# Kernel optimization log

Measured on AMD Instinct MI355X. Metric: run time of the kernel, lower is better.

The kernel has to match this reference:

```python
import jax, jax.numpy as jnp
import numpy as np
import math

N, S, R = 1, 128, 256
CM, CZ, C, MSA_H, PAIR_H, CTM, FF = 256, 128, 32, 8, 4, 128, 4
SCALE = 1.0 / math.sqrt(C)


def _ln(x, w, b):
    m = jnp.mean(x, -1, keepdims=True)
    v = jnp.var(x, -1, keepdims=True)
    return (x - m) / jnp.sqrt(v + 1e-5) * w + b


def _gated_attn(x, gate_w, qkv_w, out_w, head, bias=None):
    # x: [n, s, r, cin]; attention over r within each (n, s, head)
    n, s, r, _ = x.shape
    gate = jax.nn.sigmoid(x @ gate_w).reshape(n, s, r, head, C)
    qkv = (x @ qkv_w).reshape(n, s, r, 3, head, C)
    q, k, v = qkv[..., 0, :, :], qkv[..., 1, :, :], qkv[..., 2, :, :]
    sim = jax.nn.softmax(jnp.einsum('nsqhc,nskhc->nshqk', q, k) * SCALE, axis=-1)
    if bias is not None:
        sim = sim + bias  # NOTE: source adds bias AFTER softmax; kept faithful
    att = jnp.einsum('nshqk,nskhc->nsqhc', sim, v) * gate
    return att.reshape(n, s, r, head * C) @ out_w


def _tri_mul(x, n1w, n1b, n2w, n2b, p1, p2, p3, p4, p5, p6, incoming):
    xn = _ln(x, n1w, n1b)
    a = jax.nn.sigmoid(xn @ p1) * (xn @ p2)
    b = jax.nn.sigmoid(xn @ p3) * (xn @ p4)
    if incoming:
        p = jnp.einsum('nrsk,nrtk->nstk', a, b)
        g = jnp.swapaxes(jax.nn.sigmoid(xn @ p6), 1, 2)
    else:
        p = jnp.einsum('nsrk,ntrk->nstk', a, b)
        g = jax.nn.sigmoid(xn @ p6)
    return (_ln(p, n2w, n2b) @ p5) * g


def setup_inputs() -> dict:
    keys = iter(jax.random.split(jax.random.key(0), 80))

    def rn(shape, scale=0.02):
        return jax.random.normal(next(keys), shape, dtype=jnp.float32) * scale

    ones = lambda n: jnp.ones((n,), jnp.float32)
    zeros = lambda n: jnp.zeros((n,), jnp.float32)
    d = dict(
        msa_repr=rn((N, S, R, CM), 1.0),
        pair_repr=rn((N, R, R, CZ), 1.0),
        row_norm_m_w=ones(CM), row_norm_m_b=zeros(CM),
        row_norm_z_w=ones(CZ), row_norm_z_b=zeros(CZ),
        row_gate=rn((CM, MSA_H * C)), row_qkv=rn((CM, 3 * MSA_H * C)),
        row_out=rn((MSA_H * C, CM)), row_bias=rn((CZ, MSA_H)),
        col_norm_w=ones(CM), col_norm_b=zeros(CM),
        col_gate=rn((CM, MSA_H * C)), col_qkv=rn((CM, 3 * MSA_H * C)),
        col_out=rn((MSA_H * C, CM)),
        mt_norm_w=ones(CM), mt_norm_b=zeros(CM),
        mt_p1=rn((CM, FF * CM)), mt_p2=rn((FF * CM, CM)),
        outer_norm_w=ones(CM), outer_norm_b=zeros(CM),
        outer_p1=rn((CM, C)), outer_p2=rn((CM, C)), outer_out=rn((C * C, CZ)),
        tmo_n1_w=ones(CZ), tmo_n1_b=zeros(CZ), tmo_n2_w=ones(CTM), tmo_n2_b=zeros(CTM),
        tmo_p1=rn((CZ, CTM)), tmo_p2=rn((CZ, CTM)), tmo_p3=rn((CZ, CTM)), tmo_p4=rn((CZ, CTM)),
        tmo_p5=rn((CTM, CZ)), tmo_p6=rn((CZ, CZ)),
        tmi_n1_w=ones(CZ), tmi_n1_b=zeros(CZ), tmi_n2_w=ones(CTM), tmi_n2_b=zeros(CTM),
        tmi_p1=rn((CZ, CTM)), tmi_p2=rn((CZ, CTM)), tmi_p3=rn((CZ, CTM)), tmi_p4=rn((CZ, CTM)),
        tmi_p5=rn((CTM, CZ)), tmi_p6=rn((CZ, CZ)),
        tas_norm_w=ones(CZ), tas_norm_b=zeros(CZ),
        tas_gate=rn((CZ, PAIR_H * C)), tas_qkv=rn((CZ, 3 * PAIR_H * C)),
        tas_out=rn((PAIR_H * C, CZ)), tas_bias=rn((CZ, PAIR_H)),
        tae_norm_w=ones(CZ), tae_norm_b=zeros(CZ),
        tae_gate=rn((CZ, PAIR_H * C)), tae_qkv=rn((CZ, 3 * PAIR_H * C)),
        tae_out=rn((PAIR_H * C, CZ)), tae_bias=rn((CZ, PAIR_H)),
        pt_norm_w=ones(CZ), pt_norm_b=zeros(CZ),
        pt_p1=rn((CZ, FF * CZ)), pt_p2=rn((FF * CZ, CZ)),
    )
    return d


def reference(msa_repr, pair_repr, row_norm_m_w, row_norm_m_b, row_norm_z_w, row_norm_z_b, row_gate, row_qkv, row_out, row_bias, col_norm_w, col_norm_b, col_gate, col_qkv, col_out, mt_norm_w, mt_norm_b, mt_p1, mt_p2, outer_norm_w, outer_norm_b, outer_p1, outer_p2, outer_out, tmo_n1_w, tmo_n1_b, tmo_n2_w, tmo_n2_b, tmo_p1, tmo_p2, tmo_p3, tmo_p4, tmo_p5, tmo_p6, tmi_n1_w, tmi_n1_b, tmi_n2_w, tmi_n2_b, tmi_p1, tmi_p2, tmi_p3, tmi_p4, tmi_p5, tmi_p6, tas_norm_w, tas_norm_b, tas_gate, tas_qkv, tas_out, tas_bias, tae_norm_w, tae_norm_b, tae_gate, tae_qkv, tae_out, tae_bias, pt_norm_w, pt_norm_b, pt_p1, pt_p2):
    msa, pair = msa_repr, pair_repr
    # 1. MSA row attention with pair bias
    xm = _ln(msa, row_norm_m_w, row_norm_m_b)
    xz = _ln(pair, row_norm_z_w, row_norm_z_b)
    bias = jnp.transpose(xz @ row_bias, (0, 3, 1, 2))[:, None]  # [N,1,H,R,R]
    msa = msa + _gated_attn(xm, row_gate, row_qkv, row_out, MSA_H, bias)
    # 2. MSA column attention
    xm = _ln(msa, col_norm_w, col_norm_b)
    msa = msa + jnp.swapaxes(_gated_attn(jnp.swapaxes(xm, 1, 2), col_gate, col_qkv, col_out, MSA_H), 1, 2)
    # 3. MSA transition
    xm = _ln(msa, mt_norm_w, mt_norm_b)
    msa = msa + jax.nn.relu(xm @ mt_p1) @ mt_p2
    # 4. outer product mean (no division in source; sum over s)
    xm = _ln(msa, outer_norm_w, outer_norm_b)
    a = jnp.swapaxes(xm @ outer_p1, 1, 2)  # [n,r,s,c]
    b = jnp.swapaxes(xm @ outer_p2, 1, 2)  # [n,t,s,c]
    outer = jnp.einsum('nrsc,ntse->nrtce', a, b).reshape(a.shape[0], a.shape[1], b.shape[1], C * C)
    pair = pair + outer @ outer_out
    # 5/6. triangle multiplicative updates (outgoing then incoming)
    pair = pair + _tri_mul(pair, tmo_n1_w, tmo_n1_b, tmo_n2_w, tmo_n2_b, tmo_p1, tmo_p2, tmo_p3, tmo_p4, tmo_p5, tmo_p6, False)
    pair = pair + _tri_mul(pair, tmi_n1_w, tmi_n1_b, tmi_n2_w, tmi_n2_b, tmi_p1, tmi_p2, tmi_p3, tmi_p4, tmi_p5, tmi_p6, True)
    # 7. triangle attention (node start)
    xz = _ln(pair, tas_norm_w, tas_norm_b)
    bias = jnp.transpose(xz @ tas_bias, (0, 1, 3, 2))[:, :, :, None, :]  # [N,S,H,1,R]
    pair = pair + _gated_attn(xz, tas_gate, tas_qkv, tas_out, PAIR_H, bias)
    # 8. triangle attention (node end): transpose residue axes
    xz = jnp.swapaxes(_ln(pair, tae_norm_w, tae_norm_b), 1, 2)
    bias = jnp.transpose(xz @ tae_bias, (0, 1, 3, 2))[:, :, :, None, :]
    pair = pair + jnp.swapaxes(_gated_attn(xz, tae_gate, tae_qkv, tae_out, PAIR_H, bias), 1, 2)
    # 9. pair transition
    xz = _ln(pair, pt_norm_w, pt_norm_b)
    pair = pair + jax.nn.relu(xz @ pt_p1) @ pt_p2
    return msa, pair
```

## Files before the change

kernel.cpp:

```cpp
#include <hip/hip_runtime.h>
#include <hip/hip_bf16.h>
#include <stdint.h>

typedef __hip_bfloat16 bf16;
typedef __attribute__((ext_vector_type(4))) int   i32x4;
typedef __attribute__((ext_vector_type(4))) float f32x4;


__device__ __forceinline__ float toF(float x){ return x; }
__device__ __forceinline__ float toF(bf16 x){ return __bfloat162float(x); }
__device__ __forceinline__ bf16  toB(float x){ return __float2bfloat16(x); }

__device__ __forceinline__ void gload16(const bf16* g, bf16* l){
    __builtin_amdgcn_global_load_lds((const __attribute__((address_space(1))) void*)g,
                                     (__attribute__((address_space(3))) void*)l, 16, 0, 0);
}

#define NW_IN 58
struct WStage {
    const void* src[NW_IN];
    int off[NW_IN];
    int K[NW_IN], N[NW_IN];
};
__global__ __launch_bounds__(256) void cvt_all_k(WStage t, bf16* __restrict__ base,
                                                 const uint32_t* __restrict__ probe){
    bool isbf = (probe[0] == 0x3F803F80u);
    const int wi = blockIdx.y;
    const void* in = t.src[wi];
    bf16* out = base + t.off[wi];
    const int K = t.K[wi], N = t.N[wi];
    const int total = K ? K*N : N;
    for (int i = blockIdx.x*256 + threadIdx.x; i < total; i += gridDim.x*256){
        float v = isbf ? toF(((const bf16*)in)[i]) : ((const float*)in)[i];
        if (K){ int k = i / N, n = i - k*N; out[(size_t)n*K + k] = toB(v); }
        else    out[i] = toB(v);
    }
}
__global__ void in2f_k(const void* __restrict__ in, float* __restrict__ out, int n,
                       const uint32_t* __restrict__ probe){
    bool isbf = (probe[0] == 0x3F803F80u);
    int i = blockIdx.x*256 + threadIdx.x;
    if (i < n) out[i] = isbf ? toF(((const bf16*)in)[i]) : ((const float*)in)[i];
}

template<typename T>
__global__ void ln_k(const T* __restrict__ x, const bf16* __restrict__ w, const bf16* __restrict__ b,
                     bf16* __restrict__ out, int D){
    int row = blockIdx.x, c = threadIdx.x;
    float v = toF(x[(size_t)row*D + c]);
    float s1 = v, s2 = v*v;
    #pragma unroll
    for (int o=32;o>0;o>>=1){ s1 += __shfl_down(s1,o); s2 += __shfl_down(s2,o); }
    __shared__ float r1[4], r2[4];
    int lane = c & 63, wid = c >> 6;
    if (lane==0){ r1[wid]=s1; r2[wid]=s2; }
    __syncthreads();
    int nw = blockDim.x >> 6;
    float m=0.f, q=0.f;
    for (int i=0;i<nw;i++){ m+=r1[i]; q+=r2[i]; }
    m /= (float)D; q = q/(float)D - m*m;
    float inv = rsqrtf(q + 1e-5f);
    out[(size_t)row*D + c] = toB((v-m)*inv*toF(w[c]) + toF(b[c]));
}

template<int MODE, int HN>
__global__ __launch_bounds__(256) void bproj_k(const bf16* __restrict__ xz, const bf16* __restrict__ Wb,
                                               float* __restrict__ outb){
    __shared__ float WbS[128*HN];
    const int i = blockIdx.x, t = threadIdx.x;
    for (int idx = t; idx < 128*HN; idx += 256) WbS[idx] = toF(Wb[idx]);
    __syncthreads();
    const bf16* row = xz + ((size_t)i*256 + t)*128;
    float d[HN] = {};
    #pragma unroll 4
    for (int c8 = 0; c8 < 16; ++c8){
        uint4 v = *(const uint4*)(row + c8*8);
        bf16 tmp[8]; *(uint4*)tmp = v;
        #pragma unroll
        for (int u=0;u<8;u++){
            float x = toF(tmp[u]);
            #pragma unroll
            for (int h=0;h<HN;h++) d[h] += x * WbS[(c8*8+u)*HN + h];
        }
    }
    #pragma unroll
    for (int h=0;h<HN;h++){
        size_t idx = (MODE==0) ? ((size_t)h*65536 + (size_t)i*256 + t)
                   : (MODE==1) ? ((size_t)(i*HN+h)*256 + t)
                               : ((size_t)(t*HN+h)*256 + i);
        outb[idx] = d[h];
    }
}

template<int ACT, int MUL, int RES, int HM>
__global__ __launch_bounds__(256) void mgemm_k(const bf16* __restrict__ A, const bf16* __restrict__ Bt,
                                               bf16* __restrict__ C, float* __restrict__ Res,
                                               const bf16* __restrict__ Mul,
                                               int M, int N, int K, int lda, size_t astep,
                                               int ldbt, size_t ldc, int res_off, int gtrans){
    __shared__ alignas(16) bf16 As[128*32];
    __shared__ alignas(16) bf16 Bs[128*32];
    const int tid  = threadIdx.x;
    const int m0   = blockIdx.y << 7, n0 = blockIdx.x << 7;
    const int lane = tid & 63, w = tid >> 6;
    const int wr   = (w >> 1) << 6, wc = (w & 1) << 6;
    const int fr   = lane & 15, fq = lane >> 4;
    const int sr = tid >> 2, sc = (tid & 3) << 3;
    const bf16* ga = A  + (size_t)(m0 + sr)*lda  + sc;
    const bf16* gb = Bt + (size_t)(n0 + sr)*ldbt + sc;
    bf16* la = As + tid*8;
    bf16* lb = Bs + tid*8;
    const size_t gaS = (size_t)64*lda, gbS = (size_t)64*ldbt;

    f32x4 acc[4][4] = {};
    for (int k0=0; k0<K; k0+=32){
        gload16(ga, la);        gload16(ga + gaS, la + 2048);
        gload16(gb, lb);        gload16(gb + gbS, lb + 2048);
        ga += astep; gb += 32;
        __syncthreads();
        i32x4 af[4], bv[4];
        #pragma unroll
        for (int i=0;i<4;i++) af[i] = *(const i32x4*)(As + ((wr + i*16 + fr) << 5) + (fq << 3));
        #pragma unroll
        for (int j=0;j<4;j++) bv[j] = *(const i32x4*)(Bs + ((wc + j*16 + fr) << 5) + (fq << 3));
        #pragma unroll
        for (int i=0;i<4;i++)
            #pragma unroll
            for (int j=0;j<4;j++)
                asm("v_mfma_f32_16x16x32_bf16 %0, %1, %2, %0"
                    : "+v"(acc[i][j]) : "v"(af[i]), "v"(bv[j]));
        __syncthreads();
    }
    #pragma unroll
    for (int i=0;i<4;i++){
        const int mB = m0 + wr + i*16 + (fq << 2);
        #pragma unroll
        for (int j=0;j<4;j++){
            const int n = n0 + wc + j*16 + fr;
            #pragma unroll
            for (int r=0;r<4;r++){
                int m = mB + r;
                float x = acc[i][j][r];
                if (ACT==1) x = 1.f/(1.f + __expf(-x));
                else if (ACT==2) x = fmaxf(x, 0.f);
                if (MUL){
                    int mr = gtrans ? (((m & 255) << 8) | (m >> 8)) : m;
                    x *= toF(Mul[(size_t)mr*N + n]);
                }
                if (RES) Res[(size_t)(m + res_off)*N + n] += x;
                else if (HM) C[(size_t)(n>>5)*ldc + (size_t)m*32 + (n&31)] = toB(x);
                else     C[(size_t)m*ldc + n] = toB(x);
            }
        }
    }
}

template<int ACT, int MUL, int RES, int GATE, int MHM>
__global__ __launch_bounds__(256) void sgemm_k(const bf16* __restrict__ A,
        const bf16* __restrict__ Bt1, const bf16* __restrict__ Bt2,
        bf16* __restrict__ C, float* __restrict__ Res, const bf16* __restrict__ Mul,
        int M, int lda, int ldbt, int ldc, size_t ldmul, int res_off, int gtrans){
    __shared__ alignas(16) bf16 Bs1[128*128];
    __shared__ alignas(16) bf16 Bs2[GATE ? 128*128 : 16];
    const int tid = threadIdx.x;
    for (int idx = tid; idx < 2048; idx += 256){
        int n = idx >> 4, cc = idx & 15;
        int sc = (cc ^ (n & 15)) << 3;
        *(uint4*)(Bs1 + n*128 + sc) = *(const uint4*)(Bt1 + (size_t)n*ldbt + (cc<<3));
        if (GATE)
            *(uint4*)(Bs2 + n*128 + sc) = *(const uint4*)(Bt2 + (size_t)n*ldbt + (cc<<3));
    }
    __syncthreads();
    const int lane = tid & 63, w = tid >> 6;
    const int fr = lane & 15, fq = lane >> 4;
    const int mb = blockIdx.x*128 + w*32;
    f32x4 acc[2][8] = {};
    f32x4 acc2[2][8] = {};
    #pragma unroll
    for (int k0=0;k0<4;k0++){
        i32x4 af[2];
        #pragma unroll
        for (int i=0;i<2;i++)
            af[i] = *(const i32x4*)(A + (size_t)(mb + i*16 + fr)*lda + k0*32 + fq*8);
        const int co = ((k0*4 + fq) ^ fr) << 3;
        #pragma unroll
        for (int j=0;j<8;j++){
            i32x4 bf1 = *(const i32x4*)(Bs1 + (j*16+fr)*128 + co);
            #pragma unroll
            for (int i=0;i<2;i++)
                asm("v_mfma_f32_16x16x32_bf16 %0, %1, %2, %0"
                    : "+v"(acc[i][j]) : "v"(af[i]), "v"(bf1));
            if (GATE){
                i32x4 bf2 = *(const i32x4*)(Bs2 + (j*16+fr)*128 + co);
                #pragma unroll
                for (int i=0;i<2;i++)
                    asm("v_mfma_f32_16x16x32_bf16 %0, %1, %2, %0"
                        : "+v"(acc2[i][j]) : "v"(af[i]), "v"(bf2));
            }
        }
    }
    #pragma unroll
    for (int i=0;i<2;i++){
        #pragma unroll
        for (int j=0;j<8;j++){
            const int n = j*16 + fr;
            #pragma unroll
            for (int r=0;r<4;r++){
                int m = mb + i*16 + (fq<<2) + r;
                float x = acc[i][j][r];
                if (GATE) x = acc2[i][j][r] / (1.f + __expf(-x));
                else if (ACT==1) x = 1.f/(1.f + __expf(-x));
                else if (ACT==2) x = fmaxf(x, 0.f);
                if (MUL){
                    int mr = gtrans ? (((m & 255) << 8) | (m >> 8)) : m;
                    if (MHM) x *= toF(Mul[(size_t)(n>>5)*ldmul + (size_t)mr*32 + (n&31)]);
                    else     x *= toF(Mul[(size_t)mr*ldmul + n]);
                }
                if (RES) Res[(size_t)(m + res_off)*128 + n] += x;
                else     C[(size_t)m*ldc + n] = toB(x);
            }
        }
    }
}

__global__ __launch_bounds__(256) void btrimul_k(const bf16* __restrict__ aT, const bf16* __restrict__ bT,
                                                 bf16* __restrict__ pT){
    __shared__ alignas(16) bf16 As[128*32];
    __shared__ alignas(16) bf16 Bs[128*32];
    const int tid  = threadIdx.x;
    const int m0   = blockIdx.y << 7, n0 = blockIdx.x << 7;
    const size_t zb = (size_t)blockIdx.z << 16;
    const int lane = tid & 63, w = tid >> 6;
    const int wr   = (w >> 1) << 6, wc = (w & 1) << 6;
    const int fr   = lane & 15, fq = lane >> 4;
    const int sr = tid >> 2, sc = (tid & 3) << 3;
    const bf16* ga = aT + zb + (size_t)(m0 + sr)*256 + sc;
    const bf16* gb = bT + zb + (size_t)(n0 + sr)*256 + sc;
    bf16* la = As + tid*8;
    bf16* lb = Bs + tid*8;
    const size_t gS = (size_t)64*256;

    f32x4 acc[4][4] = {};
    for (int k0=0; k0<256; k0+=32){
        gload16(ga, la);        gload16(ga + gS, la + 2048);
        gload16(gb, lb);        gload16(gb + gS, lb + 2048);
        ga += 32; gb += 32;
        __syncthreads();
        i32x4 af[4], bv[4];
        #pragma unroll
        for (int i=0;i<4;i++) af[i] = *(const i32x4*)(As + ((wr + i*16 + fr) << 5) + (fq << 3));
        #pragma unroll
        for (int j=0;j<4;j++) bv[j] = *(const i32x4*)(Bs + ((wc + j*16 + fr) << 5) + (fq << 3));
        #pragma unroll
        for (int i=0;i<4;i++)
            #pragma unroll
            for (int j=0;j<4;j++)
                asm("v_mfma_f32_16x16x32_bf16 %0, %1, %2, %0"
                    : "+v"(acc[i][j]) : "v"(af[i]), "v"(bv[j]));
        __syncthreads();
    }
    #pragma unroll
    for (int i=0;i<4;i++){
        const int mB = m0 + wr + i*16 + (fq << 2);
        #pragma unroll
        for (int j=0;j<4;j++){
            const int n = n0 + wc + j*16 + fr;
            #pragma unroll
            for (int r=0;r<4;r++)
                pT[zb + (size_t)(mB + r)*256 + n] = toB(acc[i][j][r]);
        }
    }
}

__global__ __launch_bounds__(256) void rc2k_k(const bf16* __restrict__ in, bf16* __restrict__ out, int swap){
    __shared__ uint16_t T[128][137];
    const int tt = blockIdx.x, tid = threadIdx.x;
    size_t base_pp, out_off; int ppstride;
    if (!swap){ base_pp = (size_t)tt*128;                  ppstride = 1;   out_off = (size_t)tt*128; }
    else      { int J = tt>>1, I0 = (tt&1)*128;
                base_pp = (size_t)I0*256 + J;              ppstride = 256; out_off = (size_t)J*256 + I0; }
    for (int it=0; it<8; ++it){
        int idx = tid + it*256;
        int r = idx >> 4, c8 = (idx & 15) << 3;
        uint4 v = *(const uint4*)(in + (base_pp + (size_t)r*ppstride)*128 + c8);
        uint16_t tmp[8]; *(uint4*)tmp = v;
        #pragma unroll
        for (int t=0;t<8;t++) T[r][c8+t] = tmp[t];
    }
    __syncthreads();
    for (int it=0; it<8; ++it){
        int idx = tid + it*256;
        int k = idx >> 4, r8 = (idx & 15) << 3;
        uint16_t tmp[8];
        #pragma unroll
        for (int t=0;t<8;t++) tmp[t] = T[r8+t][k];
        *(uint4*)(out + (size_t)k*65536 + out_off + r8) = *(uint4*)tmp;
    }
}
__global__ __launch_bounds__(256) void k2rc_k(const bf16* __restrict__ in, bf16* __restrict__ out){
    __shared__ uint16_t T[128][137];
    const int tt = blockIdx.x, tid = threadIdx.x;
    const size_t a0 = (size_t)tt*128;
    for (int it=0; it<8; ++it){
        int idx = tid + it*256;
        int k = idx >> 4, r8 = (idx & 15) << 3;
        uint4 v = *(const uint4*)(in + (size_t)k*65536 + a0 + r8);
        uint16_t tmp[8]; *(uint4*)tmp = v;
        #pragma unroll
        for (int t=0;t<8;t++) T[r8+t][k] = tmp[t];
    }
    __syncthreads();
    for (int it=0; it<8; ++it){
        int idx = tid + it*256;
        int r = idx >> 4, c8 = (idx & 15) << 3;
        uint16_t tmp[8];
        #pragma unroll
        for (int t=0;t<8;t++) tmp[t] = T[r][c8+t];
        *(uint4*)(out + (a0 + r)*128 + c8) = *(uint4*)tmp;
    }
}

template<int ACT, int MUL, int RES>
__global__ __launch_bounds__(256) void gemm_k(const bf16* __restrict__ A, const bf16* __restrict__ Bw,
                                              bf16* __restrict__ C, float* __restrict__ Res,
                                              const bf16* __restrict__ Mul,
                                              int M, int N, int K, int ldb, int res_off, int gtrans){
    __shared__ float As[64][33];
    __shared__ float Bs[32][65];
    int tid = threadIdx.x;
    int m0 = blockIdx.y*64, n0 = blockIdx.x*64;
    int tx = tid & 15, ty = tid >> 4;
    float acc[4][4] = {};
    for (int k0=0; k0<K; k0+=32){
        for (int i=tid; i<64*32; i+=256){
            int r = i>>5, cc = i&31;
            As[r][cc] = toF(A[(size_t)(m0+r)*K + k0 + cc]);
        }
        for (int i=tid; i<32*64; i+=256){
            int r = i>>6, cc = i&63; int col = n0+cc;
            Bs[r][cc] = (col < N) ? toF(Bw[(size_t)(k0+r)*ldb + col]) : 0.f;
        }
        __syncthreads();
        #pragma unroll 8
        for (int k=0;k<32;k++){
            float a4[4], b4[4];
            #pragma unroll
            for (int i=0;i<4;i++) a4[i] = As[ty*4+i][k];
            #pragma unroll
            for (int j=0;j<4;j++) b4[j] = Bs[k][tx*4+j];
            #pragma unroll
            for (int i=0;i<4;i++)
                #pragma unroll
                for (int j=0;j<4;j++) acc[i][j] += a4[i]*b4[j];
        }
        __syncthreads();
    }
    #pragma unroll
    for (int i=0;i<4;i++){
        int m = m0 + ty*4 + i;
        #pragma unroll
        for (int j=0;j<4;j++){
            int n = n0 + tx*4 + j;
            if (n >= N) continue;
            float x = acc[i][j];
            if (ACT==1) x = 1.f/(1.f + __expf(-x));
            else if (ACT==2) x = fmaxf(x, 0.f);
            if (MUL){
                int mr = gtrans ? (((m & 255) << 8) | (m >> 8)) : m;
                x *= toF(Mul[(size_t)mr*N + n]);
            }
            if (RES) Res[(size_t)(m + res_off)*N + n] += x;
            else     C[(size_t)m*N + n] = toB(x);
        }
    }
}

template<int BIAS, int L>
__global__ __launch_bounds__(256) void attn4_k(bf16* __restrict__ QO,
                                               const bf16* __restrict__ Kp, const bf16* __restrict__ Vp,
                                               const float* __restrict__ bias,
                                               int H, size_t HS, int sO, int sL){
    constexpr int MW  = L/4;
    constexpr int IFR = MW/16;
    constexpr int KC  = 32;
    constexpr int NCH = L/KC;
    constexpr int VP  = L + 8;
    __shared__ alignas(16) bf16 VT_lds[32*VP];
    __shared__ alignas(16) bf16 P_lds[L*40];
    __shared__ float red[8*32 + 32];
    const int o = blockIdx.y, h = blockIdx.x, tid = threadIdx.x;
    const int lane = tid & 63, w = tid >> 6;
    const int fr = lane & 15, fq = lane >> 4;
    const size_t hb = (size_t)h*HS;

    for (int idx = tid; idx < L*4; idx += 256){
        int l = idx >> 2, c8 = (idx & 3) << 3;
        size_t p = hb + (size_t)(o*sO + l*sL)*32 + c8;
        uint4 vv = *(const uint4*)(Vp + p);
        bf16 tmp[8]; *(uint4*)tmp = vv;
        #pragma unroll
        for (int t=0;t<8;t++) VT_lds[(c8+t)*VP + l] = tmp[t];
    }
    __syncthreads();

    float* ObS = red + 256;
    if (BIAS == 2){
        int c = tid & 31, g = tid >> 5;
        const float* bp = bias + (size_t)(o*H + h)*256;
        float p = 0.f;
        for (int k = g*(L/8); k < (g+1)*(L/8); ++k)
            p += bp[k] * toF(VT_lds[c*VP + k]);
        red[g*32 + c] = p;
        __syncthreads();
        if (tid < 32){
            float s = 0.f;
            #pragma unroll
            for (int g2=0; g2<8; ++g2) s += red[g2*32 + tid];
            ObS[tid] = s;
        }
        __syncthreads();
    }

    i32x4 qf[IFR];
    #pragma unroll
    for (int i=0;i<IFR;i++){
        int q = w*MW + i*16 + fr;
        qf[i] = *(const i32x4*)(QO + hb + (size_t)(o*sO + q*sL)*32 + fq*8);
    }
    const bf16* kbase = Kp + hb + (size_t)o*sO*32 + fq*8 + (size_t)fr*sL*32;
    const size_t kstep = (size_t)sL*32;

    bf16* Pw = P_lds + w*MW*40;
    f32x4 accO[IFR][2] = {};
    f32x4 accB[IFR][2] = {};
    float lsum[IFR][4] = {};

    for (int ch=0; ch<NCH; ++ch){
        const int k0 = ch*KC;
        f32x4 sa[IFR][2] = {};
        i32x4 kf[2];
        #pragma unroll
        for (int j=0;j<2;j++) kf[j] = *(const i32x4*)(kbase + (size_t)(k0 + j*16)*kstep);
        #pragma unroll
        for (int i=0;i<IFR;i++)
            #pragma unroll
            for (int j=0;j<2;j++)
                asm("v_mfma_f32_16x16x32_bf16 %0, %1, %2, %0"
                    : "+v"(sa[i][j]) : "v"(qf[i]), "v"(kf[j]));
        #pragma unroll
        for (int i=0;i<IFR;i++)
            #pragma unroll
            for (int j=0;j<2;j++)
                #pragma unroll
                for (int r=0;r<4;r++){
                    float e = __expf(sa[i][j][r] * 0.17677669529663687f);
                    lsum[i][r] += e;
                    Pw[(i*16 + fq*4 + r)*40 + j*16 + fr] = toB(e);
                }
        i32x4 vf[2];
        #pragma unroll
        for (int j=0;j<2;j++) vf[j] = *(const i32x4*)(VT_lds + (j*16 + fr)*VP + k0 + fq*8);
        #pragma unroll
        for (int i=0;i<IFR;i++){
            i32x4 pa = *(const i32x4*)(Pw + (i*16 + fr)*40 + fq*8);
            #pragma unroll
            for (int j=0;j<2;j++)
                asm("v_mfma_f32_16x16x32_bf16 %0, %1, %2, %0"
                    : "+v"(accO[i][j]) : "v"(pa), "v"(vf[j]));
        }
        if (BIAS == 1){
            #pragma unroll
            for (int it=0; it<32; ++it){
                int q = it*2 + (lane>>5), kk = lane&31;
                Pw[q*40 + kk] = toB(bias[(size_t)h*65536 + (size_t)(w*MW + q)*256 + k0 + kk]);
            }
            #pragma unroll
            for (int i=0;i<IFR;i++){
                i32x4 pa = *(const i32x4*)(Pw + (i*16 + fr)*40 + fq*8);
                #pragma unroll
                for (int j=0;j<2;j++)
                    asm("v_mfma_f32_16x16x32_bf16 %0, %1, %2, %0"
                        : "+v"(accB[i][j]) : "v"(pa), "v"(vf[j]));
            }
        }
    }
    #pragma unroll
    for (int i=0;i<IFR;i++)
        #pragma unroll
        for (int r=0;r<4;r++){
            float s = lsum[i][r];
            s += __shfl_xor(s, 1); s += __shfl_xor(s, 2);
            s += __shfl_xor(s, 4); s += __shfl_xor(s, 8);
            lsum[i][r] = 1.f / s;
        }
    #pragma unroll
    for (int i=0;i<IFR;i++)
        #pragma unroll
        for (int j=0;j<2;j++)
            #pragma unroll
            for (int r=0;r<4;r++){
                int q = w*MW + i*16 + fq*4 + r;
                int c = j*16 + fr;
                float v = accO[i][j][r]*lsum[i][r];
                if (BIAS==1) v += accB[i][j][r];
                if (BIAS==2) v += ObS[c];
                QO[hb + (size_t)(o*sO + q*sL)*32 + c] = toB(v);
            }
}

__global__ void mulsigHM_k(bf16* __restrict__ a, const bf16* __restrict__ g, size_t HS, int NC, int n){
    int i = blockIdx.x*256 + threadIdx.x;
    if (i < n){
        int m = i / NC, col = i - m*NC;
        int h = col >> 5, c = col & 31;
        size_t o = (size_t)h*HS + (size_t)m*32 + c;
        float sg = 1.f/(1.f + __expf(-toF(g[(size_t)m*NC + col])));
        a[o] = toB(toF(a[o]) * sg);
    }
}

__global__ __launch_bounds__(256) void outer_k(const bf16* __restrict__ ap, const bf16* __restrict__ bp,
                                               bf16* __restrict__ outc, int r0){
    int t = blockIdx.x, rl = blockIdx.y, r = r0 + rl;
    __shared__ float As[128*32], Bs[128*32];
    for (int idx=threadIdx.x; idx<128*32; idx+=256){
        int s = idx>>5, c = idx&31;
        As[idx] = toF(ap[((size_t)s*256 + r)*32 + c]);
        Bs[idx] = toF(bp[((size_t)s*256 + t)*32 + c]);
    }
    __syncthreads();
    int ce0 = threadIdx.x*4;
    int c = ce0 >> 5, e0 = ce0 & 31;
    float acc[4] = {0.f,0.f,0.f,0.f};
    for (int s=0;s<128;s++){
        float av = As[s*32 + c];
        #pragma unroll
        for (int j=0;j<4;j++) acc[j] += av*Bs[s*32 + e0 + j];
    }
    size_t row = (size_t)rl*256 + t;
    #pragma unroll
    for (int j=0;j<4;j++) outc[row*1024 + ce0 + j] = toB(acc[j]);
}

static bool tshape(int i, int& K, int& N){
    switch(i){
        case 6: case 8: case 12: case 14: K=256; N=256;  return true;
        case 7: case 13:                  K=256; N=768;  return true;
        case 17:                          K=256; N=1024; return true;
        case 18:                          K=1024;N=256;  return true;
        case 23:                          K=1024;N=128;  return true;
        case 47: case 53:                 K=128; N=384;  return true;
        case 58:                          K=128; N=512;  return true;
        case 59:                          K=512; N=128;  return true;
        default:
            if ((i>=28&&i<=33)||(i>=38&&i<=43)||i==46||i==48||i==52||i==54){ K=128; N=128; return true; }
            return false;
    }
}

extern "C" void kernel_launch(void* const* d_in, const int* in_sizes, int n_in,
                              void* d_out, int out_size, void* d_ws, size_t ws_size,
                              hipStream_t stream){
    (void)n_in; (void)out_size; (void)ws_size;
    const int MSA_N  = 128*256*256;
    const int PAIR_N = 256*256*128;
    const size_t HSm = (size_t)32768*32;
    const size_t HSp = (size_t)65536*32;
    const uint32_t* probe = (const uint32_t*)d_in[2];

    char*  w     = (char*)d_ws;
    bf16*  wsts  = (bf16*)(w);
    float* biasF = (float*)(w + 4194304);
    bf16*  lnb   = (bf16*)(w + 6291456);
    bf16*  bufA  = (bf16*)(w + 23068672);
    bf16*  bufB  = (bf16*)(w + 39845888);
    bf16*  bufC  = (bf16*)(w + 56623104);

    float* msaF  = (float*)d_out;
    float* pairF = msaF + MSA_N;

    size_t woff[64]; { size_t acc = 0;
        for (int i=2;i<60;i++){ woff[i] = acc; acc += ((size_t)in_sizes[i] + 63) & ~(size_t)63; } }
    #define W(i) (wsts + woff[i])

    {
        WStage st;
        for (int i=2;i<60;i++){
            int tk, tn;
            st.src[i-2] = d_in[i];
            st.off[i-2] = (int)woff[i];
            if (tshape(i, tk, tn)){ st.K[i-2]=tk; st.N[i-2]=tn; }
            else                   { st.K[i-2]=0;  st.N[i-2]=in_sizes[i]; }
        }
        cvt_all_k<<<dim3(64, NW_IN),256,0,stream>>>(st, wsts, probe);
    }

    in2f_k<<<32768,256,0,stream>>>(d_in[0], msaF,  MSA_N,  probe);
    in2f_k<<<32768,256,0,stream>>>(d_in[1], pairF, PAIR_N, probe);

    ln_k<float><<<32768,256,0,stream>>>(msaF, W(2), W(3), lnb, 256);
    ln_k<float><<<65536,128,0,stream>>>(pairF, W(4), W(5), bufC, 128);
    bproj_k<0,8><<<256,256,0,stream>>>(bufC, W(9), biasF);
    mgemm_k<0,0,0,1><<<dim3(6,256),256,0,stream>>>(lnb, W(7), bufA, nullptr, nullptr,
                                                   32768,768,256, 256,32,256, HSm, 0,0);
    attn4_k<1,256><<<dim3(8,128),256,0,stream>>>(bufA, bufA+8*HSm, bufA+16*HSm, biasF, 8, HSm, 256, 1);
    mgemm_k<0,0,0,0><<<dim3(2,256),256,0,stream>>>(lnb, W(6), bufA+8*HSm, nullptr, nullptr,
                                                   32768,256,256, 256,32,256, 256, 0,0);
    mulsigHM_k<<<32768,256,0,stream>>>(bufA, bufA+8*HSm, HSm, 256, MSA_N);
    mgemm_k<0,0,1,0><<<dim3(2,256),256,0,stream>>>(bufA, W(8), nullptr, msaF, nullptr,
                                                   32768,256,256, 32,HSm,256, 256, 0,0);

    ln_k<float><<<32768,256,0,stream>>>(msaF, W(10), W(11), lnb, 256);
    mgemm_k<0,0,0,1><<<dim3(6,256),256,0,stream>>>(lnb, W(13), bufA, nullptr, nullptr,
                                                   32768,768,256, 256,32,256, HSm, 0,0);
    attn4_k<0,128><<<dim3(8,256),256,0,stream>>>(bufA, bufA+8*HSm, bufA+16*HSm, nullptr, 8, HSm, 1, 256);
    mgemm_k<0,0,0,0><<<dim3(2,256),256,0,stream>>>(lnb, W(12), bufA+8*HSm, nullptr, nullptr,
                                                   32768,256,256, 256,32,256, 256, 0,0);
    mulsigHM_k<<<32768,256,0,stream>>>(bufA, bufA+8*HSm, HSm, 256, MSA_N);
    mgemm_k<0,0,1,0><<<dim3(2,256),256,0,stream>>>(bufA, W(14), nullptr, msaF, nullptr,
                                                   32768,256,256, 32,HSm,256, 256, 0,0);

    ln_k<float><<<32768,256,0,stream>>>(msaF, W(15), W(16), lnb, 256);
    for (int ch=0; ch<4; ++ch){
        mgemm_k<2,0,0,0><<<dim3(2,256),256,0,stream>>>(lnb, W(17)+ch*65536, bufA, nullptr, nullptr,
                                                       32768,256,256, 256,32,256, 256, 0,0);
        mgemm_k<0,0,1,0><<<dim3(2,256),256,0,stream>>>(bufA, W(18)+ch*256, nullptr, msaF, nullptr,
                                                       32768,256,256, 256,32,1024, 256, 0,0);
    }

    ln_k<float><<<32768,256,0,stream>>>(msaF, W(19), W(20), lnb, 256);
    gemm_k<0,0,0><<<dim3(1,512),256,0,stream>>>(lnb, W(21), bufA, nullptr, nullptr, 32768,32,256, 32, 0,0);
    gemm_k<0,0,0><<<dim3(1,512),256,0,stream>>>(lnb, W(22), bufB, nullptr, nullptr, 32768,32,256, 32, 0,0);
    for (int ch=0; ch<8; ++ch){
        outer_k<<<dim3(256,32),256,0,stream>>>(bufA, bufB, lnb, ch*32);
        mgemm_k<0,0,1,0><<<dim3(1,64),256,0,stream>>>(lnb, W(23), nullptr, pairF, nullptr,
                                                      8192,128,1024, 1024,32,1024, 128, ch*8192,0);
    }

    for (int tm=0; tm<2; ++tm){
        int o = tm ? 34 : 24;
        int inc = tm;
        ln_k<float><<<65536,128,0,stream>>>(pairF, W(o+0), W(o+1), lnb, 128);
        sgemm_k<0,0,0,1,0><<<512,256,0,stream>>>(lnb, W(o+4), W(o+5), bufA, nullptr, nullptr,
                                                 65536, 128,128,128,0, 0,0);
        sgemm_k<0,0,0,1,0><<<512,256,0,stream>>>(lnb, W(o+6), W(o+7), bufB, nullptr, nullptr,
                                                 65536, 128,128,128,0, 0,0);
        rc2k_k<<<512,256,0,stream>>>(bufA, bufC, inc);
        rc2k_k<<<512,256,0,stream>>>(bufB, bufA, inc);
        btrimul_k<<<dim3(2,2,128),256,0,stream>>>(bufC, bufA, bufB);
        k2rc_k<<<512,256,0,stream>>>(bufB, bufC);
        ln_k<bf16><<<65536,128,0,stream>>>(bufC, W(o+2), W(o+3), bufC, 128);
        sgemm_k<1,0,0,0,0><<<512,256,0,stream>>>(lnb, W(o+9), nullptr, bufA, nullptr, nullptr,
                                                 65536, 128,128,128,0, 0,0);
        sgemm_k<0,1,1,0,0><<<512,256,0,stream>>>(bufC, W(o+8), nullptr, nullptr, pairF, bufA,
                                                 65536, 128,128,0,128, 0, inc);
    }

    ln_k<float><<<65536,128,0,stream>>>(pairF, W(44), W(45), lnb, 128);
    bproj_k<1,4><<<256,256,0,stream>>>(lnb, W(49), biasF);
    mgemm_k<0,0,0,1><<<dim3(3,512),256,0,stream>>>(lnb, W(47), bufA, nullptr, nullptr,
                                                   65536,384,128, 128,32,128, HSp, 0,0);
    attn4_k<2,256><<<dim3(4,256),256,0,stream>>>(bufA, bufA+4*HSp, bufA+8*HSp, biasF, 4, HSp, 256, 1);
    sgemm_k<1,1,0,0,1><<<512,256,0,stream>>>(lnb, W(46), nullptr, bufA+4*HSp, nullptr, bufA,
                                             65536, 128,128,128, HSp, 0,0);
    sgemm_k<0,0,1,0,0><<<512,256,0,stream>>>(bufA+4*HSp, W(48), nullptr, nullptr, pairF, nullptr,
                                             65536, 128,128,0,0, 0,0);
    ln_k<float><<<65536,128,0,stream>>>(pairF, W(50), W(51), lnb, 128);
    bproj_k<2,4><<<256,256,0,stream>>>(lnb, W(55), biasF);
    mgemm_k<0,0,0,1><<<dim3(3,512),256,0,stream>>>(lnb, W(53), bufA, nullptr, nullptr,
                                                   65536,384,128, 128,32,128, HSp, 0,0);
    attn4_k<2,256><<<dim3(4,256),256,0,stream>>>(bufA, bufA+4*HSp, bufA+8*HSp, biasF, 4, HSp, 1, 256);
    sgemm_k<1,1,0,0,1><<<512,256,0,stream>>>(lnb, W(52), nullptr, bufA+4*HSp, nullptr, bufA,
                                             65536, 128,128,128, HSp, 0,0);
    sgemm_k<0,0,1,0,0><<<512,256,0,stream>>>(bufA+4*HSp, W(54), nullptr, nullptr, pairF, nullptr,
                                             65536, 128,128,0,0, 0,0);

    ln_k<float><<<65536,128,0,stream>>>(pairF, W(56), W(57), lnb, 128);
    for (int ch=0; ch<4; ++ch){
        sgemm_k<2,0,0,0,0><<<512,256,0,stream>>>(lnb, W(58)+ch*16384, nullptr, bufA, nullptr, nullptr,
                                                 65536, 128,128,128,0, 0,0);
        sgemm_k<0,0,1,0,0><<<512,256,0,stream>>>(bufA, W(59)+ch*128, nullptr, nullptr, pairF, nullptr,
                                                 65536, 128,512,0,0, 0,0);
    }
}
```

Measured before the change: 2.481 ms.

## Stage K in LDS, transpose score MFMA, store bias as bf16 in attention

The attention kernel now stages K into LDS alongside V instead of reading K fragments from global memory on every chunk. The score MFMA operands are swapped so each lane holds four consecutive keys for one query. That allows packed bf16 conversion, 8-byte stores into a padded transposed P buffer, and a row sum that needs only two cross-lane shuffles. The bias projection is now written as bf16 and loaded directly as an MFMA operand, which removes the scalar LDS round-trip for the row-attention bias. This costs extra LDS per block and some bias precision, and may reduce occupancy.

Result: faster. 2.412 ms (-2.8%).

```diff
diff --git a/kernel.cpp b/kernel.cpp
--- a/kernel.cpp
+++ b/kernel.cpp
@@ -4,6 +4,7 @@
 
 typedef __hip_bfloat16 bf16;
 typedef __attribute__((ext_vector_type(4))) int   i32x4;
+typedef __attribute__((ext_vector_type(2))) unsigned u32x2;
 typedef __attribute__((ext_vector_type(4))) float f32x4;
 
 
@@ -65,7 +66,7 @@
 
 template<int MODE, int HN>
 __global__ __launch_bounds__(256) void bproj_k(const bf16* __restrict__ xz, const bf16* __restrict__ Wb,
-                                               float* __restrict__ outb){
+                                               bf16* __restrict__ outb){
     __shared__ float WbS[128*HN];
     const int i = blockIdx.x, t = threadIdx.x;
     for (int idx = t; idx < 128*HN; idx += 256) WbS[idx] = toF(Wb[idx]);
@@ -88,7 +89,7 @@
         size_t idx = (MODE==0) ? ((size_t)h*65536 + (size_t)i*256 + t)
                    : (MODE==1) ? ((size_t)(i*HN+h)*256 + t)
                                : ((size_t)(t*HN+h)*256 + i);
-        outb[idx] = d[h];
+        outb[idx] = toB(d[h]);
     }
 }
 
@@ -378,15 +379,17 @@
 template<int BIAS, int L>
 __global__ __launch_bounds__(256) void attn4_k(bf16* __restrict__ QO,
                                                const bf16* __restrict__ Kp, const bf16* __restrict__ Vp,
-                                               const float* __restrict__ bias,
+                                               const bf16* __restrict__ bias,
                                                int H, size_t HS, int sO, int sL){
     constexpr int MW  = L/4;
     constexpr int IFR = MW/16;
     constexpr int KC  = 32;
     constexpr int NCH = L/KC;
     constexpr int VP  = L + 8;
+    constexpr int PTW = 44;
+    __shared__ alignas(16) bf16 K_lds[L*40];
     __shared__ alignas(16) bf16 VT_lds[32*VP];
-    __shared__ alignas(16) bf16 P_lds[L*40];
+    __shared__ alignas(16) bf16 PT_lds[4*MW*PTW];
     __shared__ float red[8*32 + 32];
     const int o = blockIdx.y, h = blockIdx.x, tid = threadIdx.x;
     const int lane = tid & 63, w = tid >> 6;
@@ -396,6 +399,7 @@
     for (int idx = tid; idx < L*4; idx += 256){
         int l = idx >> 2, c8 = (idx & 3) << 3;
         size_t p = hb + (size_t)(o*sO + l*sL)*32 + c8;
+        *(uint4*)(K_lds + l*40 + c8) = *(const uint4*)(Kp + p);
         uint4 vv = *(const uint4*)(Vp + p);
         bf16 tmp[8]; *(uint4*)tmp = vv;
         #pragma unroll
@@ -406,10 +410,10 @@
     float* ObS = red + 256;
     if (BIAS == 2){
         int c = tid & 31, g = tid >> 5;
-        const float* bp = bias + (size_t)(o*H + h)*256;
+        const bf16* bp = bias + (size_t)(o*H + h)*256;
         float p = 0.f;
         for (int k = g*(L/8); k < (g+1)*(L/8); ++k)
-            p += bp[k] * toF(VT_lds[c*VP + k]);
+            p += toF(bp[k]) * toF(VT_lds[c*VP + k]);
         red[g*32 + c] = p;
         __syncthreads();
         if (tid < 32){
@@ -427,42 +431,45 @@
         int q = w*MW + i*16 + fr;
         qf[i] = *(const i32x4*)(QO + hb + (size_t)(o*sO + q*sL)*32 + fq*8);
     }
-    const bf16* kbase = Kp + hb + (size_t)o*sO*32 + fq*8 + (size_t)fr*sL*32;
-    const size_t kstep = (size_t)sL*32;
-
-    bf16* Pw = P_lds + w*MW*40;
+    bf16* Pw = PT_lds + w*MW*PTW;
     f32x4 accO[IFR][2] = {};
     f32x4 accB[IFR][2] = {};
-    float lsum[IFR][4] = {};
+    float ls[IFR] = {};
 
     for (int ch=0; ch<NCH; ++ch){
         const int k0 = ch*KC;
         f32x4 sa[IFR][2] = {};
         i32x4 kf[2];
         #pragma unroll
-        for (int j=0;j<2;j++) kf[j] = *(const i32x4*)(kbase + (size_t)(k0 + j*16)*kstep);
+        for (int j=0;j<2;j++) kf[j] = *(const i32x4*)(K_lds + (k0 + j*16 + fr)*40 + fq*8);
         #pragma unroll
         for (int i=0;i<IFR;i++)
             #pragma unroll
             for (int j=0;j<2;j++)
                 asm("v_mfma_f32_16x16x32_bf16 %0, %1, %2, %0"
-                    : "+v"(sa[i][j]) : "v"(qf[i]), "v"(kf[j]));
-        #pragma unroll
-        for (int i=0;i<IFR;i++)
-            #pragma unroll
-            for (int j=0;j<2;j++)
-                #pragma unroll
-                for (int r=0;r<4;r++){
-                    float e = __expf(sa[i][j][r] * 0.17677669529663687f);
-                    lsum[i][r] += e;
-                    Pw[(i*16 + fq*4 + r)*40 + j*16 + fr] = toB(e);
-                }
+                    : "+v"(sa[i][j]) : "v"(kf[j]), "v"(qf[i]));
+        #pragma unroll
+        for (int i=0;i<IFR;i++){
+            #pragma unroll
+            for (int j=0;j<2;j++){
+                float e0 = __expf(sa[i][j][0] * 0.17677669529663687f);
+                float e1 = __expf(sa[i][j][1] * 0.17677669529663687f);
+                float e2 = __expf(sa[i][j][2] * 0.17677669529663687f);
+                float e3 = __expf(sa[i][j][3] * 0.17677669529663687f);
+                ls[i] += (e0+e1) + (e2+e3);
+                unsigned d0, d1;
+                asm("v_cvt_pk_bf16_f32 %0, %1, %2" : "=v"(d0) : "v"(e0), "v"(e1));
+                asm("v_cvt_pk_bf16_f32 %0, %1, %2" : "=v"(d1) : "v"(e2), "v"(e3));
+                u32x2 dd = {d0, d1};
+                *(u32x2*)(Pw + (i*16 + fr)*PTW + j*16 + fq*4) = dd;
+            }
+        }
         i32x4 vf[2];
         #pragma unroll
         for (int j=0;j<2;j++) vf[j] = *(const i32x4*)(VT_lds + (j*16 + fr)*VP + k0 + fq*8);
         #pragma unroll
         for (int i=0;i<IFR;i++){
-            i32x4 pa = *(const i32x4*)(Pw + (i*16 + fr)*40 + fq*8);
+            i32x4 pa = *(const i32x4*)(Pw + (i*16 + fr)*PTW + fq*8);
             #pragma unroll
             for (int j=0;j<2;j++)
                 asm("v_mfma_f32_16x16x32_bf16 %0, %1, %2, %0"
@@ -470,29 +477,22 @@
         }
         if (BIAS == 1){
             #pragma unroll
-            for (int it=0; it<32; ++it){
-                int q = it*2 + (lane>>5), kk = lane&31;
-                Pw[q*40 + kk] = toB(bias[(size_t)h*65536 + (size_t)(w*MW + q)*256 + k0 + kk]);
-            }
-            #pragma unroll
             for (int i=0;i<IFR;i++){
-                i32x4 pa = *(const i32x4*)(Pw + (i*16 + fr)*40 + fq*8);
+                i32x4 ba = *(const i32x4*)(bias + (size_t)h*65536
+                               + (size_t)(w*MW + i*16 + fr)*256 + k0 + fq*8);
                 #pragma unroll
                 for (int j=0;j<2;j++)
                     asm("v_mfma_f32_16x16x32_bf16 %0, %1, %2, %0"
-                        : "+v"(accB[i][j]) : "v"(pa), "v"(vf[j]));
+                        : "+v"(accB[i][j]) : "v"(ba), "v"(vf[j]));
             }
         }
     }
     #pragma unroll
-    for (int i=0;i<IFR;i++)
-        #pragma unroll
-        for (int r=0;r<4;r++){
-            float s = lsum[i][r];
-            s += __shfl_xor(s, 1); s += __shfl_xor(s, 2);
-            s += __shfl_xor(s, 4); s += __shfl_xor(s, 8);
-            lsum[i][r] = 1.f / s;
-        }
+    for (int i=0;i<IFR;i++){
+        float s = ls[i];
+        s += __shfl_xor(s, 16); s += __shfl_xor(s, 32);
+        ls[i] = 1.f / s;
+    }
     #pragma unroll
     for (int i=0;i<IFR;i++)
         #pragma unroll
@@ -501,7 +501,8 @@
             for (int r=0;r<4;r++){
                 int q = w*MW + i*16 + fq*4 + r;
                 int c = j*16 + fr;
-                float v = accO[i][j][r]*lsum[i][r];
+                float inv = __shfl(ls[i], fq*4 + r);
+                float v = accO[i][j][r]*inv;
                 if (BIAS==1) v += accB[i][j][r];
                 if (BIAS==2) v += ObS[c];
                 QO[hb + (size_t)(o*sO + q*sL)*32 + c] = toB(v);
@@ -570,7 +571,7 @@
 
     char*  w     = (char*)d_ws;
     bf16*  wsts  = (bf16*)(w);
-    float* biasF = (float*)(w + 4194304);
+    bf16*  biasB = (bf16*)(w + 4194304);
     bf16*  lnb   = (bf16*)(w + 6291456);
     bf16*  bufA  = (bf16*)(w + 23068672);
     bf16*  bufB  = (bf16*)(w + 39845888);
@@ -600,10 +601,10 @@
 
     ln_k<float><<<32768,256,0,stream>>>(msaF, W(2), W(3), lnb, 256);
     ln_k<float><<<65536,128,0,stream>>>(pairF, W(4), W(5), bufC, 128);
-    bproj_k<0,8><<<256,256,0,stream>>>(bufC, W(9), biasF);
+    bproj_k<0,8><<<256,256,0,stream>>>(bufC, W(9), biasB);
     mgemm_k<0,0,0,1><<<dim3(6,256),256,0,stream>>>(lnb, W(7), bufA, nullptr, nullptr,
                                                    32768,768,256, 256,32,256, HSm, 0,0);
-    attn4_k<1,256><<<dim3(8,128),256,0,stream>>>(bufA, bufA+8*HSm, bufA+16*HSm, biasF, 8, HSm, 256, 1);
+    attn4_k<1,256><<<dim3(8,128),256,0,stream>>>(bufA, bufA+8*HSm, bufA+16*HSm, biasB, 8, HSm, 256, 1);
     mgemm_k<0,0,0,0><<<dim3(2,256),256,0,stream>>>(lnb, W(6), bufA+8*HSm, nullptr, nullptr,
                                                    32768,256,256, 256,32,256, 256, 0,0);
     mulsigHM_k<<<32768,256,0,stream>>>(bufA, bufA+8*HSm, HSm, 256, MSA_N);
@@ -657,19 +658,19 @@
     }
 
     ln_k<float><<<65536,128,0,stream>>>(pairF, W(44), W(45), lnb, 128);
-    bproj_k<1,4><<<256,256,0,stream>>>(lnb, W(49), biasF);
+    bproj_k<1,4><<<256,256,0,stream>>>(lnb, W(49), biasB);
     mgemm_k<0,0,0,1><<<dim3(3,512),256,0,stream>>>(lnb, W(47), bufA, nullptr, nullptr,
                                                    65536,384,128, 128,32,128, HSp, 0,0);
-    attn4_k<2,256><<<dim3(4,256),256,0,stream>>>(bufA, bufA+4*HSp, bufA+8*HSp, biasF, 4, HSp, 256, 1);
+    attn4_k<2,256><<<dim3(4,256),256,0,stream>>>(bufA, bufA+4*HSp, bufA+8*HSp, biasB, 4, HSp, 256, 1);
     sgemm_k<1,1,0,0,1><<<512,256,0,stream>>>(lnb, W(46), nullptr, bufA+4*HSp, nullptr, bufA,
                                              65536, 128,128,128, HSp, 0,0);
     sgemm_k<0,0,1,0,0><<<512,256,0,stream>>>(bufA+4*HSp, W(48), nullptr, nullptr, pairF, nullptr,
                                              65536, 128,128,0,0, 0,0);
     ln_k<float><<<65536,128,0,stream>>>(pairF, W(50), W(51), lnb, 128);
-    bproj_k<2,4><<<256,256,0,stream>>>(lnb, W(55), biasF);
+    bproj_k<2,4><<<256,256,0,stream>>>(lnb, W(55), biasB);
     mgemm_k<0,0,0,1><<<dim3(3,512),256,0,stream>>>(lnb, W(53), bufA, nullptr, nullptr,
                                                    65536,384,128, 128,32,128, HSp, 0,0);
-    attn4_k<2,256><<<dim3(4,256),256,0,stream>>>(bufA, bufA+4*HSp, bufA+8*HSp, biasF, 4, HSp, 1, 256);
+    attn4_k<2,256><<<dim3(4,256),256,0,stream>>>(bufA, bufA+4*HSp, bufA+8*HSp, biasB, 4, HSp, 1, 256);
     sgemm_k<1,1,0,0,1><<<512,256,0,stream>>>(lnb, W(52), nullptr, bufA+4*HSp, nullptr, bufA,
                                              65536, 128,128,128, HSp, 0,0);
     sgemm_k<0,0,1,0,0><<<512,256,0,stream>>>(bufA+4*HSp, W(54), nullptr, nullptr, pairF, nullptr,
```
